# Optimization experiments

Measured on AMD Instinct MI355X. Metric: run time of the kernel, lower is better.

The kernel has to match this reference:

```python
import jax, jax.numpy as jnp
import numpy as np

NEG_INF = -9e15  # matches the torch -9000000000000000.0 mask value
LRELU_SLOPE = 0.01  # torch nn.LeakyReLU default


def setup_inputs() -> dict:
    key = jax.random.key(0)
    k1, k2, k3, k4 = jax.random.split(key, 4)
    N, F_in, F_out = 8192, 256, 128
    x = jax.random.normal(k1, (N, F_in), dtype=jnp.float32)
    adj = jax.random.randint(k2, (N, N), 0, 2, dtype=jnp.int32)
    # xavier_uniform with gain=1.414
    limW = 1.414 * np.sqrt(6.0 / (F_in + F_out))
    W = jax.random.uniform(k3, (F_in, F_out), minval=-limW, maxval=limW, dtype=jnp.float32)
    lima = 1.414 * np.sqrt(6.0 / (2 * F_out + 1))
    a = jax.random.uniform(k4, (2 * F_out, 1), minval=-lima, maxval=lima, dtype=jnp.float32)
    return {"x": x, "adj": adj, "W": W, "a": a}


def reference(x, adj, W, a):
    # h: [N, F_out]
    h = x @ W
    F_out = h.shape[1]
    a1 = a[:F_out, 0]   # attention vector for source node i
    a2 = a[F_out:, 0]   # attention vector for target node j
    # e[i, j] = leaky_relu(h_i . a1 + h_j . a2) -- equivalent to the repeat/cat
    # construction without materializing the [N, N, 2F] tensor.
    e = (h @ a1)[:, None] + (h @ a2)[None, :]  # [N, N]
    e = jnp.where(e > 0, e, LRELU_SLOPE * e)
    scores = jnp.where(adj > 0, e, NEG_INF)
    attention = jax.nn.softmax(scores, axis=1)  # dropout omitted (eval mode)
    h_prime = attention @ h  # [N, F_out]
    return jax.nn.elu(h_prime)
```

## Files before the change

### kernel.cpp

```cpp
#include <hip/hip_runtime.h>
#include <hip/hip_bf16.h>
#include <stdint.h>


#define N_NODES 8192
#define F_INF   256
#define F_OUT   128
#define LRELU   0.01f

typedef __bf16 bf16x8 __attribute__((ext_vector_type(8)));
typedef float  f32x4  __attribute__((ext_vector_type(4)));
using bf16 = __hip_bfloat16;

__device__ __forceinline__ float b2f(bf16 v) { return __bfloat162float(v); }
__device__ __forceinline__ bf16  f2b(float v) { return __float2bfloat16(v); }

__global__ __launch_bounds__(256) void k_xw(const float* __restrict__ x,
                                            const float* __restrict__ W,
                                            const float* __restrict__ a,
                                            bf16* __restrict__ hT,
                                            float* __restrict__ s1,
                                            float* __restrict__ s2) {
    __shared__ __align__(16) bf16 WTh[F_OUT][F_INF + 8];
    __shared__ __align__(16) bf16 WTl[F_OUT][F_INF + 8];
    __shared__ __align__(16) bf16 XSh[32][72];
    __shared__ __align__(16) bf16 XSl[32][72];
    __shared__ float a1s[F_OUT], a2s[F_OUT], s1L[32], s2L[32];
    const int tid  = threadIdx.x;
    const int lane = tid & 63, wave = tid >> 6;
    const int i0   = blockIdx.x * 32;
    if (tid < F_OUT) { a1s[tid] = a[tid]; a2s[tid] = a[tid + F_OUT]; }
    if (tid < 32)    { s1L[tid] = 0.f; s2L[tid] = 0.f; }
    for (int idx = tid; idx < (F_INF * F_OUT) / 8; idx += 256) {
        int k  = idx >> 4;
        int n0 = (idx & 15) * 8;
        const float* src = W + (size_t)k * F_OUT + n0;
        float4 va = *(const float4*)(src);
        float4 vb = *(const float4*)(src + 4);
        float v[8] = {va.x, va.y, va.z, va.w, vb.x, vb.y, vb.z, vb.w};
#pragma unroll
        for (int c = 0; c < 8; ++c) {
            bf16 hi = f2b(v[c]);
            WTh[n0 + c][k] = hi;
            WTl[n0 + c][k] = f2b(v[c] - b2f(hi));
        }
    }
    __syncthreads();
    f32x4 acc[4];
#pragma unroll
    for (int t = 0; t < 4; ++t) acc[t] = {0.f, 0.f, 0.f, 0.f};
    const int m = lane & 15, quad = lane >> 4;
    const int rt = wave & 1, cH = wave >> 1;
    for (int kc = 0; kc < F_INF / 64; ++kc) {
        const int k0 = kc * 64;
        {
            int part = tid & 7;
            int r    = tid >> 3;
            const float* src = x + (size_t)(i0 + r) * F_INF + k0 + part * 8;
            float4 va = *(const float4*)(src);
            float4 vb = *(const float4*)(src + 4);
            float v[8] = {va.x, va.y, va.z, va.w, vb.x, vb.y, vb.z, vb.w};
            __align__(16) bf16 th[8];
            __align__(16) bf16 tl[8];
#pragma unroll
            for (int c = 0; c < 8; ++c) {
                bf16 hi = f2b(v[c]);
                th[c] = hi;
                tl[c] = f2b(v[c] - b2f(hi));
            }
            *(uint4*)(&XSh[r][part * 8]) = *(const uint4*)th;
            *(uint4*)(&XSl[r][part * 8]) = *(const uint4*)tl;
        }
        __syncthreads();
#pragma unroll
        for (int ks = 0; ks < 2; ++ks) {
            bf16x8 ah = *(const bf16x8*)(&XSh[rt * 16 + m][ks * 32 + quad * 8]);
            bf16x8 al = *(const bf16x8*)(&XSl[rt * 16 + m][ks * 32 + quad * 8]);
#pragma unroll
            for (int c = 0; c < 4; ++c) {
                const int ct = cH * 4 + c;
                bf16x8 bh = *(const bf16x8*)(&WTh[ct * 16 + m][k0 + ks * 32 + quad * 8]);
                bf16x8 bl = *(const bf16x8*)(&WTl[ct * 16 + m][k0 + ks * 32 + quad * 8]);
                acc[c] = __builtin_amdgcn_mfma_f32_16x16x32_bf16(al, bh, acc[c], 0, 0, 0);
                acc[c] = __builtin_amdgcn_mfma_f32_16x16x32_bf16(ah, bl, acc[c], 0, 0, 0);
                acc[c] = __builtin_amdgcn_mfma_f32_16x16x32_bf16(ah, bh, acc[c], 0, 0, 0);
            }
        }
        __syncthreads();
    }
    float p1[4] = {0.f, 0.f, 0.f, 0.f}, p2[4] = {0.f, 0.f, 0.f, 0.f};
#pragma unroll
    for (int c = 0; c < 4; ++c) {
        const int f = (cH * 4 + c) * 16 + m;
        const float w1 = a1s[f], w2 = a2s[f];
#pragma unroll
        for (int r = 0; r < 4; ++r) { p1[r] += acc[c][r] * w1; p2[r] += acc[c][r] * w2; }
    }
#pragma unroll
    for (int r = 0; r < 4; ++r) {
        const int row = rt * 16 + quad * 4 + r;
        atomicAdd(&s1L[row], p1[r]);
        atomicAdd(&s2L[row], p2[r]);
    }
#pragma unroll
    for (int c = 0; c < 4; ++c) {
        const int f = (cH * 4 + c) * 16 + m;
#pragma unroll
        for (int r = 0; r < 4; ++r) {
            const int i = i0 + rt * 16 + quad * 4 + r;
            hT[(size_t)f * N_NODES + i] = f2b(acc[c][r]);
        }
    }
    __syncthreads();
    if (tid < 32) { s1[i0 + tid] = s1L[tid]; s2[i0 + tid] = s2L[tid]; }
}

__global__ __launch_bounds__(256) void k_max(const float* __restrict__ s2,
                                             float* __restrict__ mg) {
    __shared__ float red[256];
    int tid = threadIdx.x;
    float m = -1e30f;
    for (int j = tid; j < N_NODES; j += 256) m = fmaxf(m, s2[j]);
    red[tid] = m;
    __syncthreads();
    for (int s = 128; s > 0; s >>= 1) {
        if (tid < s) red[tid] = fmaxf(red[tid], red[tid + s]);
        __syncthreads();
    }
    if (tid == 0) mg[0] = red[0];
}

__global__ __launch_bounds__(256, 4) void k_attn(const int* __restrict__ adj,
                                                 const float* __restrict__ s1g,
                                                 const float* __restrict__ s2g,
                                                 const float* __restrict__ mg,
                                                 const bf16* __restrict__ hT,
                                                 float* __restrict__ Of,
                                                 float* __restrict__ lp) {
    __shared__ __align__(16) bf16 HS[F_OUT][72];
    __shared__ float s2s[2048];
    __shared__ float lsum[32];
    const int tid  = threadIdx.x;
    const int lane = tid & 63, wave = tid >> 6;
    const int m = lane & 15, quad = lane >> 4;
    const int rt = wave & 1, kh = wave >> 1;
    const int i0    = blockIdx.x * 32;
    const int jq    = blockIdx.y;
    const int jbase = jq * 2048;
    const int irow  = i0 + rt * 16 + m;
    const float s1v = s1g[irow];
    const float tmi = s1v + mg[0];
    const float mi  = fmaxf(tmi, LRELU * tmi);
    if (tid < 32) lsum[tid] = 0.f;
    for (int c = tid; c < 2048 / 4; c += 256)
        *(float4*)&s2s[c * 4] = *(const float4*)(s2g + jbase + c * 4);
    const int part = tid & 7, fr = tid >> 3;
    const bf16* hTp = hT + jbase + part * 8;
    {
        uint4 v0 = *(const uint4*)(hTp + (size_t)(fr +  0) * N_NODES);
        uint4 v1 = *(const uint4*)(hTp + (size_t)(fr + 32) * N_NODES);
        uint4 v2 = *(const uint4*)(hTp + (size_t)(fr + 64) * N_NODES);
        uint4 v3 = *(const uint4*)(hTp + (size_t)(fr + 96) * N_NODES);
        *(uint4*)&HS[fr +  0][part * 8] = v0;
        *(uint4*)&HS[fr + 32][part * 8] = v1;
        *(uint4*)&HS[fr + 64][part * 8] = v2;
        *(uint4*)&HS[fr + 96][part * 8] = v3;
    }
    const int jloc = kh * 32 + quad * 8;
    const int4* arowp = (const int4*)(adj + (size_t)irow * N_NODES + jbase);
    int4 av0 = arowp[0 * 16 + jloc / 4];
    int4 av1 = arowp[0 * 16 + jloc / 4 + 1];
    float lacc = 0.f;
    f32x4 acc[8];
#pragma unroll
    for (int c = 0; c < 8; ++c) acc[c] = {0.f, 0.f, 0.f, 0.f};
    __syncthreads();

    for (int jc = 0; jc < 32; ++jc) {
        const int jn = (jc < 31) ? jc + 1 : 31;
        uint4 h0 = *(const uint4*)(hTp + (size_t)(fr +  0) * N_NODES + jn * 64);
        uint4 h1 = *(const uint4*)(hTp + (size_t)(fr + 32) * N_NODES + jn * 64);
        uint4 h2 = *(const uint4*)(hTp + (size_t)(fr + 64) * N_NODES + jn * 64);
        uint4 h3 = *(const uint4*)(hTp + (size_t)(fr + 96) * N_NODES + jn * 64);
        const int am[8] = {av0.x, av0.y, av0.z, av0.w, av1.x, av1.y, av1.z, av1.w};
        const float* s2p = &s2s[jc * 64 + jloc];
        __align__(16) bf16 a8[8];
#pragma unroll
        for (int t = 0; t < 8; ++t) {
            float e = s1v + s2p[t];
            e = fmaxf(e, LRELU * e);
            float w = (am[t] > 0) ? __expf(e - mi) : 0.f;
            bf16 b = f2b(w);
            a8[t] = b;
            lacc += b2f(b);
        }
        bf16x8 afrag = *(const bf16x8*)a8;
        av0 = arowp[jn * 16 + jloc / 4];
        av1 = arowp[jn * 16 + jloc / 4 + 1];
#pragma unroll
        for (int c = 0; c < 8; ++c) {
            bf16x8 bfr = *(const bf16x8*)(&HS[c * 16 + m][jloc]);
            acc[c] = __builtin_amdgcn_mfma_f32_16x16x32_bf16(afrag, bfr, acc[c], 0, 0, 0);
        }
        __syncthreads();
        *(uint4*)&HS[fr +  0][part * 8] = h0;
        *(uint4*)&HS[fr + 32][part * 8] = h1;
        *(uint4*)&HS[fr + 64][part * 8] = h2;
        *(uint4*)&HS[fr + 96][part * 8] = h3;
        __syncthreads();
    }
    lacc += __shfl_xor(lacc, 16);
    lacc += __shfl_xor(lacc, 32);
    if (quad == 0) atomicAdd(&lsum[rt * 16 + m], lacc);
    __syncthreads();
    if (tid < 32) lp[(size_t)jq * N_NODES + i0 + tid] = lsum[tid];
    float* scr = (float*)&HS[0][0];
    if (kh == 1) {
#pragma unroll
        for (int c = 0; c < 8; ++c)
#pragma unroll
            for (int r = 0; r < 4; ++r)
                scr[(rt * 16 + quad * 4 + r) * 128 + c * 16 + m] = acc[c][r];
    }
    __syncthreads();
    if (kh == 0) {
#pragma unroll
        for (int c = 0; c < 8; ++c)
#pragma unroll
            for (int r = 0; r < 4; ++r) {
                const int row = rt * 16 + quad * 4 + r;
                const int f   = c * 16 + m;
                Of[((size_t)jq * N_NODES + i0 + row) * F_OUT + f] =
                    acc[c][r] + scr[row * 128 + f];
            }
    }
}

__global__ __launch_bounds__(256) void k_comb(const float* __restrict__ Of,
                                              const float* __restrict__ lp,
                                              float* __restrict__ out) {
    size_t gid = (size_t)blockIdx.x * 256 + threadIdx.x;
    int i = (int)(gid >> 7);
    float s = 0.f, l = 0.f;
#pragma unroll
    for (int q = 0; q < 4; ++q) {
        s += Of[(size_t)q * (N_NODES * (size_t)F_OUT) + gid];
        l += lp[q * N_NODES + i];
    }
    float o = s / l;
    out[gid] = o > 0.f ? o : __expf(o) - 1.f;
}

extern "C" void kernel_launch(void* const* d_in, const int* in_sizes, int n_in,
                              void* d_out, int out_size, void* d_ws, size_t ws_size,
                              hipStream_t stream) {
    (void)out_size; (void)ws_size;
    const float* x   = nullptr;
    const int*   adj = nullptr;
    const float* W   = nullptr;
    const float* a   = nullptr;
    for (int ii = 0; ii < n_in; ++ii) {
        int sz = in_sizes[ii];
        if      (sz == N_NODES * F_INF)  x   = (const float*)d_in[ii];
        else if (sz == F_INF * F_OUT)    W   = (const float*)d_in[ii];
        else if (sz == 2 * F_OUT)        a   = (const float*)d_in[ii];
        else                             adj = (const int*)d_in[ii];
    }
    float* out = (float*)d_out;

    char* ws = (char*)d_ws;
    bf16*  hT = (bf16*)ws;  ws += (size_t)F_OUT * N_NODES * 2;
    float* s1 = (float*)ws; ws += N_NODES * 4;
    float* s2 = (float*)ws; ws += N_NODES * 4;
    float* mg = (float*)ws; ws += 256;
    float* lp = (float*)ws; ws += 4 * N_NODES * 4;
    float* Of = (float*)ws;

    k_xw  <<<N_NODES / 32, 256, 0, stream>>>(x, W, a, hT, s1, s2);
    k_max <<<1, 256, 0, stream>>>(s2, mg);
    k_attn<<<dim3(N_NODES / 32, 4), 256, 0, stream>>>(adj, s1, s2, mg, hT, Of, lp);
    k_comb<<<(N_NODES * F_OUT) / 256, 256, 0, stream>>>(Of, lp, out);
}
```

Measured before the change: 437.0 us.

## Drop split-bf16 projection, compute scores via W·a, retile attention across 8 j-splits

The x@W projection drops the hi/lo bf16 three-MFMA split and runs a single bf16 MFMA with 64-row tiles. The attention scores s1/s2 are now computed in fp32 as x·(W·a) by two new small kernels instead of being reduced from the projection accumulators. The attention kernel now gives each wave its own 16 rows over the full 64-wide j-chunk, which removes the cross-wave LDS reduction and atomics, and splits j into 8 parts so the combine kernel sums 8 partials. The goals are less MFMA work, more parallelism and fewer LDS syncs, at the cost of lower precision in h, two extra launches and more partial-output traffic.

```diff
diff --git a/kernel.cpp b/kernel.cpp
--- a/kernel.cpp
+++ b/kernel.cpp
@@ -15,22 +15,29 @@
 __device__ __forceinline__ float b2f(bf16 v) { return __bfloat162float(v); }
 __device__ __forceinline__ bf16  f2b(float v) { return __float2bfloat16(v); }
 
+__global__ __launch_bounds__(256) void k_wa(const float* __restrict__ W,
+                                            const float* __restrict__ a,
+                                            float* __restrict__ wa) {
+    const int k = threadIdx.x;
+    const float* wr = W + (size_t)k * F_OUT;
+    float v1 = 0.f, v2 = 0.f;
+    for (int f = 0; f < F_OUT; ++f) {
+        float w = wr[f];
+        v1 += w * a[f];
+        v2 += w * a[F_OUT + f];
+    }
+    wa[k] = v1;
+    wa[F_INF + k] = v2;
+}
+
 __global__ __launch_bounds__(256) void k_xw(const float* __restrict__ x,
                                             const float* __restrict__ W,
-                                            const float* __restrict__ a,
-                                            bf16* __restrict__ hT,
-                                            float* __restrict__ s1,
-                                            float* __restrict__ s2) {
-    __shared__ __align__(16) bf16 WTh[F_OUT][F_INF + 8];
-    __shared__ __align__(16) bf16 WTl[F_OUT][F_INF + 8];
-    __shared__ __align__(16) bf16 XSh[32][72];
-    __shared__ __align__(16) bf16 XSl[32][72];
-    __shared__ float a1s[F_OUT], a2s[F_OUT], s1L[32], s2L[32];
+                                            bf16* __restrict__ hT) {
+    __shared__ __align__(16) bf16 WT[F_OUT][F_INF + 8];
+    __shared__ __align__(16) bf16 XS[64][72];
     const int tid  = threadIdx.x;
     const int lane = tid & 63, wave = tid >> 6;
-    const int i0   = blockIdx.x * 32;
-    if (tid < F_OUT) { a1s[tid] = a[tid]; a2s[tid] = a[tid + F_OUT]; }
-    if (tid < 32)    { s1L[tid] = 0.f; s2L[tid] = 0.f; }
+    const int i0   = blockIdx.x * 64;
     for (int idx = tid; idx < (F_INF * F_OUT) / 8; idx += 256) {
         int k  = idx >> 4;
         int n0 = (idx & 15) * 8;
@@ -39,80 +46,76 @@
         float4 vb = *(const float4*)(src + 4);
         float v[8] = {va.x, va.y, va.z, va.w, vb.x, vb.y, vb.z, vb.w};
 #pragma unroll
-        for (int c = 0; c < 8; ++c) {
-            bf16 hi = f2b(v[c]);
-            WTh[n0 + c][k] = hi;
-            WTl[n0 + c][k] = f2b(v[c] - b2f(hi));
-        }
+        for (int c = 0; c < 8; ++c) WT[n0 + c][k] = f2b(v[c]);
     }
     __syncthreads();
-    f32x4 acc[4];
-#pragma unroll
-    for (int t = 0; t < 4; ++t) acc[t] = {0.f, 0.f, 0.f, 0.f};
+    f32x4 acc[8];
+#pragma unroll
+    for (int t = 0; t < 8; ++t) acc[t] = {0.f, 0.f, 0.f, 0.f};
     const int m = lane & 15, quad = lane >> 4;
-    const int rt = wave & 1, cH = wave >> 1;
+    const int rt = wave;
     for (int kc = 0; kc < F_INF / 64; ++kc) {
         const int k0 = kc * 64;
         {
             int part = tid & 7;
             int r    = tid >> 3;
-            const float* src = x + (size_t)(i0 + r) * F_INF + k0 + part * 8;
-            float4 va = *(const float4*)(src);
-            float4 vb = *(const float4*)(src + 4);
-            float v[8] = {va.x, va.y, va.z, va.w, vb.x, vb.y, vb.z, vb.w};
-            __align__(16) bf16 th[8];
-            __align__(16) bf16 tl[8];
-#pragma unroll
-            for (int c = 0; c < 8; ++c) {
-                bf16 hi = f2b(v[c]);
-                th[c] = hi;
-                tl[c] = f2b(v[c] - b2f(hi));
-            }
-            *(uint4*)(&XSh[r][part * 8]) = *(const uint4*)th;
-            *(uint4*)(&XSl[r][part * 8]) = *(const uint4*)tl;
+#pragma unroll
+            for (int p = 0; p < 2; ++p) {
+                int rr = r + p * 32;
+                const float* src = x + (size_t)(i0 + rr) * F_INF + k0 + part * 8;
+                float4 va = *(const float4*)(src);
+                float4 vb = *(const float4*)(src + 4);
+                float v[8] = {va.x, va.y, va.z, va.w, vb.x, vb.y, vb.z, vb.w};
+                __align__(16) bf16 th[8];
+#pragma unroll
+                for (int c = 0; c < 8; ++c) th[c] = f2b(v[c]);
+                *(uint4*)(&XS[rr][part * 8]) = *(const uint4*)th;
+            }
         }
         __syncthreads();
 #pragma unroll
         for (int ks = 0; ks < 2; ++ks) {
-            bf16x8 ah = *(const bf16x8*)(&XSh[rt * 16 + m][ks * 32 + quad * 8]);
-            bf16x8 al = *(const bf16x8*)(&XSl[rt * 16 + m][ks * 32 + quad * 8]);
-#pragma unroll
-            for (int c = 0; c < 4; ++c) {
-                const int ct = cH * 4 + c;
-                bf16x8 bh = *(const bf16x8*)(&WTh[ct * 16 + m][k0 + ks * 32 + quad * 8]);
-                bf16x8 bl = *(const bf16x8*)(&WTl[ct * 16 + m][k0 + ks * 32 + quad * 8]);
-                acc[c] = __builtin_amdgcn_mfma_f32_16x16x32_bf16(al, bh, acc[c], 0, 0, 0);
-                acc[c] = __builtin_amdgcn_mfma_f32_16x16x32_bf16(ah, bl, acc[c], 0, 0, 0);
-                acc[c] = __builtin_amdgcn_mfma_f32_16x16x32_bf16(ah, bh, acc[c], 0, 0, 0);
-            }
-        }
-        __syncthreads();
-    }
-    float p1[4] = {0.f, 0.f, 0.f, 0.f}, p2[4] = {0.f, 0.f, 0.f, 0.f};
-#pragma unroll
-    for (int c = 0; c < 4; ++c) {
-        const int f = (cH * 4 + c) * 16 + m;
-        const float w1 = a1s[f], w2 = a2s[f];
-#pragma unroll
-        for (int r = 0; r < 4; ++r) { p1[r] += acc[c][r] * w1; p2[r] += acc[c][r] * w2; }
-    }
-#pragma unroll
-    for (int r = 0; r < 4; ++r) {
-        const int row = rt * 16 + quad * 4 + r;
-        atomicAdd(&s1L[row], p1[r]);
-        atomicAdd(&s2L[row], p2[r]);
-    }
-#pragma unroll
-    for (int c = 0; c < 4; ++c) {
-        const int f = (cH * 4 + c) * 16 + m;
+            bf16x8 af = *(const bf16x8*)(&XS[rt * 16 + m][ks * 32 + quad * 8]);
+#pragma unroll
+            for (int ct = 0; ct < 8; ++ct) {
+                bf16x8 bfr = *(const bf16x8*)(&WT[ct * 16 + m][k0 + ks * 32 + quad * 8]);
+                acc[ct] = __builtin_amdgcn_mfma_f32_16x16x32_bf16(af, bfr, acc[ct], 0, 0, 0);
+            }
+        }
+        __syncthreads();
+    }
+#pragma unroll
+    for (int ct = 0; ct < 8; ++ct) {
+        const int f = ct * 16 + m;
 #pragma unroll
         for (int r = 0; r < 4; ++r) {
             const int i = i0 + rt * 16 + quad * 4 + r;
-            hT[(size_t)f * N_NODES + i] = f2b(acc[c][r]);
-        }
-    }
-    __syncthreads();
-    if (tid < 32) { s1[i0 + tid] = s1L[tid]; s2[i0 + tid] = s2L[tid]; }
+            hT[(size_t)f * N_NODES + i] = f2b(acc[ct][r]);
+        }
+    }
+}
+
+__global__ __launch_bounds__(256) void k_s12(const float* __restrict__ x,
+                                             const float* __restrict__ wa,
+                                             float* __restrict__ s1,
+                                             float* __restrict__ s2) {
+    const int tid  = threadIdx.x;
+    const int lane = tid & 63, wave = tid >> 6;
+    float4 w1 = *(const float4*)(wa + lane * 4);
+    float4 w2 = *(const float4*)(wa + F_INF + lane * 4);
+    const int ibase = (blockIdx.x * 4 + wave) * 64;
+    for (int r = 0; r < 64; ++r) {
+        const int i = ibase + r;
+        float4 xv = *(const float4*)(x + (size_t)i * F_INF + lane * 4);
+        float v1 = xv.x * w1.x + xv.y * w1.y + xv.z * w1.z + xv.w * w1.w;
+        float v2 = xv.x * w2.x + xv.y * w2.y + xv.z * w2.z + xv.w * w2.w;
+#pragma unroll
+        for (int off = 32; off >= 1; off >>= 1) {
+            v1 += __shfl_xor(v1, off);
+            v2 += __shfl_xor(v2, off);
+        }
+        if (lane == 0) { s1[i] = v1; s2[i] = v2; }
+    }
 }
 
 __global__ __launch_bounds__(256) void k_max(const float* __restrict__ s2,
@@ -138,22 +141,18 @@
                                                  float* __restrict__ Of,
                                                  float* __restrict__ lp) {
     __shared__ __align__(16) bf16 HS[F_OUT][72];
-    __shared__ float s2s[2048];
-    __shared__ float lsum[32];
+    __shared__ float s2s[1024];
     const int tid  = threadIdx.x;
     const int lane = tid & 63, wave = tid >> 6;
     const int m = lane & 15, quad = lane >> 4;
-    const int rt = wave & 1, kh = wave >> 1;
-    const int i0    = blockIdx.x * 32;
+    const int i0    = blockIdx.x * 64;
     const int jq    = blockIdx.y;
-    const int jbase = jq * 2048;
-    const int irow  = i0 + rt * 16 + m;
+    const int jbase = jq * 1024;
+    const int irow  = i0 + wave * 16 + m;
     const float s1v = s1g[irow];
     const float tmi = s1v + mg[0];
     const float mi  = fmaxf(tmi, LRELU * tmi);
-    if (tid < 32) lsum[tid] = 0.f;
-    for (int c = tid; c < 2048 / 4; c += 256)
-        *(float4*)&s2s[c * 4] = *(const float4*)(s2g + jbase + c * 4);
+    *(float4*)&s2s[tid * 4] = *(const float4*)(s2g + jbase + tid * 4);
     const int part = tid & 7, fr = tid >> 3;
     const bf16* hTp = hT + jbase + part * 8;
     {
@@ -166,42 +165,49 @@
         *(uint4*)&HS[fr + 64][part * 8] = v2;
         *(uint4*)&HS[fr + 96][part * 8] = v3;
     }
-    const int jloc = kh * 32 + quad * 8;
     const int4* arowp = (const int4*)(adj + (size_t)irow * N_NODES + jbase);
-    int4 av0 = arowp[0 * 16 + jloc / 4];
-    int4 av1 = arowp[0 * 16 + jloc / 4 + 1];
+    int4 av[4];
+    av[0] = arowp[quad * 2];     av[1] = arowp[quad * 2 + 1];
+    av[2] = arowp[8 + quad * 2]; av[3] = arowp[8 + quad * 2 + 1];
     float lacc = 0.f;
     f32x4 acc[8];
 #pragma unroll
     for (int c = 0; c < 8; ++c) acc[c] = {0.f, 0.f, 0.f, 0.f};
     __syncthreads();
 
-    for (int jc = 0; jc < 32; ++jc) {
-        const int jn = (jc < 31) ? jc + 1 : 31;
+    for (int jc = 0; jc < 16; ++jc) {
+        const int jn = (jc < 15) ? jc + 1 : 15;
         uint4 h0 = *(const uint4*)(hTp + (size_t)(fr +  0) * N_NODES + jn * 64);
         uint4 h1 = *(const uint4*)(hTp + (size_t)(fr + 32) * N_NODES + jn * 64);
         uint4 h2 = *(const uint4*)(hTp + (size_t)(fr + 64) * N_NODES + jn * 64);
         uint4 h3 = *(const uint4*)(hTp + (size_t)(fr + 96) * N_NODES + jn * 64);
-        const int am[8] = {av0.x, av0.y, av0.z, av0.w, av1.x, av1.y, av1.z, av1.w};
-        const float* s2p = &s2s[jc * 64 + jloc];
-        __align__(16) bf16 a8[8];
-#pragma unroll
-        for (int t = 0; t < 8; ++t) {
-            float e = s1v + s2p[t];
-            e = fmaxf(e, LRELU * e);
-            float w = (am[t] > 0) ? __expf(e - mi) : 0.f;
-            bf16 b = f2b(w);
-            a8[t] = b;
-            lacc += b2f(b);
-        }
-        bf16x8 afrag = *(const bf16x8*)a8;
-        av0 = arowp[jn * 16 + jloc / 4];
-        av1 = arowp[jn * 16 + jloc / 4 + 1];
-#pragma unroll
-        for (int c = 0; c < 8; ++c) {
-            bf16x8 bfr = *(const bf16x8*)(&HS[c * 16 + m][jloc]);
-            acc[c] = __builtin_amdgcn_mfma_f32_16x16x32_bf16(afrag, bfr, acc[c], 0, 0, 0);
-        }
+        bf16x8 afrag[2];
+#pragma unroll
+        for (int kh = 0; kh < 2; ++kh) {
+            const int am[8] = {av[kh*2].x, av[kh*2].y, av[kh*2].z, av[kh*2].w,
+                               av[kh*2+1].x, av[kh*2+1].y, av[kh*2+1].z, av[kh*2+1].w};
+            const float* s2p = &s2s[jc * 64 + kh * 32 + quad * 8];
+            __align__(16) bf16 a8[8];
+#pragma unroll
+            for (int t = 0; t < 8; ++t) {
+                float e = s1v + s2p[t];
+                e = fmaxf(e, LRELU * e);
+                float w = (am[t] > 0) ? __expf(e - mi) : 0.f;
+                bf16 b = f2b(w);
+                a8[t] = b;
+                lacc += b2f(b);
+            }
+            afrag[kh] = *(const bf16x8*)a8;
+        }
+        av[0] = arowp[jn * 16 + quad * 2];     av[1] = arowp[jn * 16 + quad * 2 + 1];
+        av[2] = arowp[jn * 16 + 8 + quad * 2]; av[3] = arowp[jn * 16 + 8 + quad * 2 + 1];
+#pragma unroll
+        for (int kh = 0; kh < 2; ++kh)
+#pragma unroll
+            for (int c = 0; c < 8; ++c) {
+                bf16x8 bfr = *(const bf16x8*)(&HS[c * 16 + m][kh * 32 + quad * 8]);
+                acc[c] = __builtin_amdgcn_mfma_f32_16x16x32_bf16(afrag[kh], bfr, acc[c], 0, 0, 0);
+            }
         __syncthreads();
         *(uint4*)&HS[fr +  0][part * 8] = h0;
         *(uint4*)&HS[fr + 32][part * 8] = h1;
@@ -211,28 +217,15 @@
     }
     lacc += __shfl_xor(lacc, 16);
     lacc += __shfl_xor(lacc, 32);
-    if (quad == 0) atomicAdd(&lsum[rt * 16 + m], lacc);
-    __syncthreads();
-    if (tid < 32) lp[(size_t)jq * N_NODES + i0 + tid] = lsum[tid];
-    float* scr = (float*)&HS[0][0];
-    if (kh == 1) {
-#pragma unroll
-        for (int c = 0; c < 8; ++c)
-#pragma unroll
-            for (int r = 0; r < 4; ++r)
-                scr[(rt * 16 + quad * 4 + r) * 128 + c * 16 + m] = acc[c][r];
-    }
-    __syncthreads();
-    if (kh == 0) {
-#pragma unroll
-        for (int c = 0; c < 8; ++c)
-#pragma unroll
-            for (int r = 0; r < 4; ++r) {
-                const int row = rt * 16 + quad * 4 + r;
-                const int f   = c * 16 + m;
-                Of[((size_t)jq * N_NODES + i0 + row) * F_OUT + f] =
-                    acc[c][r] + scr[row * 128 + f];
-            }
+    if (quad == 0) lp[(size_t)jq * N_NODES + irow] = lacc;
+#pragma unroll
+    for (int c = 0; c < 8; ++c) {
+        const int f = c * 16 + m;
+#pragma unroll
+        for (int r = 0; r < 4; ++r) {
+            const int i = i0 + wave * 16 + quad * 4 + r;
+            Of[((size_t)jq * N_NODES + i) * F_OUT + f] = acc[c][r];
+        }
     }
 }
 
@@ -243,7 +236,7 @@
     int i = (int)(gid >> 7);
     float s = 0.f, l = 0.f;
 #pragma unroll
-    for (int q = 0; q < 4; ++q) {
+    for (int q = 0; q < 8; ++q) {
         s += Of[(size_t)q * (N_NODES * (size_t)F_OUT) + gid];
         l += lp[q * N_NODES + i];
     }
@@ -270,14 +263,17 @@
 
     char* ws = (char*)d_ws;
     bf16*  hT = (bf16*)ws;  ws += (size_t)F_OUT * N_NODES * 2;
+    float* wa = (float*)ws; ws += 2 * F_INF * 4;
     float* s1 = (float*)ws; ws += N_NODES * 4;
     float* s2 = (float*)ws; ws += N_NODES * 4;
     float* mg = (float*)ws; ws += 256;
-    float* lp = (float*)ws; ws += 4 * N_NODES * 4;
+    float* lp = (float*)ws; ws += 8 * N_NODES * 4;
     float* Of = (float*)ws;
 
-    k_xw  <<<N_NODES / 32, 256, 0, stream>>>(x, W, a, hT, s1, s2);
+    k_wa  <<<1, 256, 0, stream>>>(W, a, wa);
+    k_xw  <<<N_NODES / 64, 256, 0, stream>>>(x, W, hT);
+    k_s12 <<<N_NODES / 256, 256, 0, stream>>>(x, wa, s1, s2);
     k_max <<<1, 256, 0, stream>>>(s2, mg);
-    k_attn<<<dim3(N_NODES / 32, 4), 256, 0, stream>>>(adj, s1, s2, mg, hT, Of, lp);
+    k_attn<<<dim3(N_NODES / 64, 8), 256, 0, stream>>>(adj, s1, s2, mg, hT, Of, lp);
     k_comb<<<(N_NODES * F_OUT) / 256, 256, 0, stream>>>(Of, lp, out);
 }
```

After: 482.1 us. 1.1x slower.
